# Kernel optimization log

Hardware: AMD Instinct MI355X
Metric: run time of the kernel (lower is better)

Reference implementation:

```python
import jax, jax.numpy as jnp
import numpy as np

N_NODES = 100000
N_EDGES = 1600000

def setup_inputs() -> dict:
    key = jax.random.key(0)
    ks = jax.random.split(key, 6)
    x = jax.random.normal(ks[0], (N_NODES, 128), dtype=jnp.float32)
    edge_index = jax.random.randint(ks[1], (2, N_EDGES), 0, N_NODES, dtype=jnp.int64)
    edge_weight = jax.random.uniform(ks[2], (N_EDGES,), dtype=jnp.float32)
    # kaiming-uniform-like init for weights, zeros for biases (as in reset_parameters)
    bound1 = float(np.sqrt(6.0 / 128))
    W1 = jax.random.uniform(ks[3], (128, 128), minval=-bound1, maxval=bound1, dtype=jnp.float32)
    b1 = jnp.zeros((128,), dtype=jnp.float32)
    W2 = jax.random.uniform(ks[4], (128, 64), minval=-bound1, maxval=bound1, dtype=jnp.float32)
    b2 = jnp.zeros((64,), dtype=jnp.float32)
    return {"x": x, "edge_index": edge_index, "edge_weight": edge_weight,
            "W1": W1, "b1": b1, "W2": W2, "b2": b2}

def _gcn_conv(x, src, dst, ew, W, b):
    support = x @ W                      # [N, F_out] dense GEMM
    msgs = ew[:, None] * support[src]    # [E, F_out] gather + scale (spmm values)
    out = jax.ops.segment_sum(msgs, dst, num_segments=N_NODES)  # scatter-add
    return out + b

def reference(x, edge_index, edge_weight, W1, b1, W2, b2):
    dst, src = edge_index[0], edge_index[1]  # adj[dst, src] = edge_weight
    h = _gcn_conv(x, src, dst, edge_weight, W1, b1)
    h = jax.nn.relu(h)
    out = _gcn_conv(h, src, dst, edge_weight, W2, b2)
    return out
```

## Files before the change

### kernel.cpp

```cpp
#include <hip/hip_runtime.h>

#define N_NODES 100000
#define N_EDGES 1600000
#define NB 391
#define PAD 16
#define SC_EPB 2048
#define SC_BLOCKS ((N_EDGES + SC_EPB - 1) / SC_EPB)
#define LDA 136
#define NTILES ((N_NODES + 127) / 128)

typedef unsigned int uint32;
typedef __attribute__((ext_vector_type(8))) short bf16x8;
typedef __attribute__((ext_vector_type(4))) float f32x4;

__device__ __forceinline__ uint32 bf16_rne(float f) {
    uint32 u = __float_as_uint(f);
    return (u + 0x7fffu + ((u >> 16) & 1u)) >> 16;
}
__device__ __forceinline__ uint32 pack_bf16x2(float lo, float hi) {
    return bf16_rne(lo) | (bf16_rne(hi) << 16);
}
__device__ __forceinline__ float bf16_lo(uint32 u) { return __uint_as_float(u << 16); }
__device__ __forceinline__ float bf16_hi(uint32 u) { return __uint_as_float(u & 0xFFFF0000u); }

__global__ __launch_bounds__(256) void conv_x(const float* __restrict__ x,
                                              uint32* __restrict__ xb) {
    const int t = blockIdx.x * 256 + threadIdx.x;
    if (t >= N_NODES * 64) return;
    const float2 v = ((const float2*)x)[t];
    xb[t] = pack_bf16x2(v.x, v.y);
}

__global__ __launch_bounds__(256) void conv_w(const float* __restrict__ W1,
                                              const float* __restrict__ W2,
                                              uint32* __restrict__ w1tb,
                                              uint32* __restrict__ w2tb) {
    const int t = blockIdx.x * 256 + threadIdx.x;
    if (t < 128 * 64) {
        const int n = t >> 6, kk = t & 63;
        w1tb[t] = pack_bf16x2(W1[(2 * kk) * 128 + n], W1[(2 * kk + 1) * 128 + n]);
    } else if (t < 128 * 64 + 64 * 64) {
        const int u = t - 128 * 64;
        const int n = u >> 6, kk = u & 63;
        w2tb[u] = pack_bf16x2(W2[(2 * kk) * 64 + n], W2[(2 * kk + 1) * 64 + n]);
    }
}

__global__ __launch_bounds__(256) void bucket_hist(const int* __restrict__ dst,
                                                   int* __restrict__ bktCnt) {
    __shared__ int h[NB];
    for (int i = threadIdx.x; i < NB; i += 256) h[i] = 0;
    __syncthreads();
    for (int e = blockIdx.x * 256 + threadIdx.x; e < N_EDGES; e += NB * 256)
        atomicAdd(&h[dst[e] >> 8], 1);
    __syncthreads();
    for (int i = threadIdx.x; i < NB; i += 256)
        if (h[i]) atomicAdd(&bktCnt[i * PAD], h[i]);
}

__global__ __launch_bounds__(512) void bucket_scan(const int* __restrict__ bktCnt,
                                                   int* __restrict__ bBase,
                                                   int* __restrict__ bCur,
                                                   int* __restrict__ offs) {
    __shared__ int s[512];
    const int t = threadIdx.x;
    int v = (t < NB) ? bktCnt[t * PAD] : 0;
    s[t] = v;
    __syncthreads();
#pragma unroll
    for (int off = 1; off < 512; off <<= 1) {
        int u = (t >= off) ? s[t - off] : 0;
        __syncthreads();
        s[t] += u;
        __syncthreads();
    }
    if (t < NB) {
        const int excl = s[t] - v;
        bBase[t] = excl;
        bCur[t * PAD] = excl;
    }
    if (t == 0) {
        bBase[NB] = N_EDGES;
        offs[N_NODES] = N_EDGES;
    }
}

__global__ __launch_bounds__(256) void bucket_scatter2(const int* __restrict__ dst,
                                                       const int* __restrict__ src,
                                                       const float* __restrict__ ew,
                                                       int* __restrict__ bCur,
                                                       int2* __restrict__ bucketed) {
    __shared__ int h[NB];
    __shared__ int cur[NB];
    const int base = blockIdx.x * SC_EPB;
    const int end  = min(base + SC_EPB, N_EDGES);

    for (int i = threadIdx.x; i < NB; i += 256) h[i] = 0;
    __syncthreads();
    for (int e = base + threadIdx.x; e < end; e += 256)
        atomicAdd(&h[dst[e] >> 8], 1);
    __syncthreads();
    for (int i = threadIdx.x; i < NB; i += 256) {
        const int c = h[i];
        cur[i] = c ? atomicAdd(&bCur[i * PAD], c) : 0;
    }
    __syncthreads();
    for (int e = base + threadIdx.x; e < end; e += 256) {
        const int d = dst[e];
        const int p = atomicAdd(&cur[d >> 8], 1);
        bucketed[p] = make_int2(src[e] | ((d & 255) << 17), __float_as_int(ew[e]));
    }
}

__global__ __launch_bounds__(256) void bucket_csr(const int2* __restrict__ bucketed,
                                                  const int* __restrict__ bBase,
                                                  int* __restrict__ offs,
                                                  int2* __restrict__ csr_ef) {
    __shared__ int sdeg[256];
    __shared__ int lcur[256];
    const int b   = blockIdx.x;
    const int t   = threadIdx.x;
    const int beg = bBase[b], end = bBase[b + 1];

    sdeg[t] = 0;
    __syncthreads();
    for (int j = beg + t; j < end; j += 256)
        atomicAdd(&sdeg[(bucketed[j].x >> 17) & 255], 1);
    __syncthreads();
    const int mydeg = sdeg[t];
#pragma unroll
    for (int off = 1; off < 256; off <<= 1) {
        int u = (t >= off) ? sdeg[t - off] : 0;
        __syncthreads();
        sdeg[t] += u;
        __syncthreads();
    }
    const int excl = sdeg[t] - mydeg;
    lcur[t] = excl;
    const int node = b * 256 + t;
    if (node < N_NODES) offs[node] = beg + excl;
    __syncthreads();

    for (int j = beg + t; j < end; j += 256) {
        const int2 v = bucketed[j];
        const int dl = (v.x >> 17) & 255;
        const int p  = beg + atomicAdd(&lcur[dl], 1);
        csr_ef[p] = make_int2(v.x & 0x1FFFF, v.y);
    }
}

template <int FEAT>
__global__ __launch_bounds__(256) void aggregate(const void* __restrict__ featv,
                                                 const int* __restrict__ offs,
                                                 const int2* __restrict__ csr_ef,
                                                 const float* __restrict__ bias,
                                                 void* __restrict__ outv) {
    const int n    = (blockIdx.x * 256 + threadIdx.x) >> 6;
    const int lane = threadIdx.x & 63;
    if (n >= N_NODES) return;
    const int beg = offs[n], end = offs[n + 1];
    const uint4* feat = (const uint4*)featv;

    float a0 = 0.f, a1 = 0.f, a2 = 0.f, a3 = 0.f;
    float a4 = 0.f, a5 = 0.f, a6 = 0.f, a7 = 0.f;

    if constexpr (FEAT == 128) {
        const int g  = lane >> 4;
        const int f8 = lane & 15;

        for (int j = beg + g; j < end; j += 8) {
            {
                const int2 e = csr_ef[j];
                const uint4 r = feat[(unsigned)(e.x * 16 + f8)];
                const float w = __int_as_float(e.y);
                a0 += w * bf16_lo(r.x); a1 += w * bf16_hi(r.x);
                a2 += w * bf16_lo(r.y); a3 += w * bf16_hi(r.y);
                a4 += w * bf16_lo(r.z); a5 += w * bf16_hi(r.z);
                a6 += w * bf16_lo(r.w); a7 += w * bf16_hi(r.w);
            }
            if (j + 4 < end) {
                const int2 e = csr_ef[j + 4];
                const uint4 r = feat[(unsigned)(e.x * 16 + f8)];
                const float w = __int_as_float(e.y);
                a0 += w * bf16_lo(r.x); a1 += w * bf16_hi(r.x);
                a2 += w * bf16_lo(r.y); a3 += w * bf16_hi(r.y);
                a4 += w * bf16_lo(r.z); a5 += w * bf16_hi(r.z);
                a6 += w * bf16_lo(r.w); a7 += w * bf16_hi(r.w);
            }
        }

        a0 += __shfl_xor(a0, 16); a1 += __shfl_xor(a1, 16);
        a2 += __shfl_xor(a2, 16); a3 += __shfl_xor(a3, 16);
        a4 += __shfl_xor(a4, 16); a5 += __shfl_xor(a5, 16);
        a6 += __shfl_xor(a6, 16); a7 += __shfl_xor(a7, 16);
        a0 += __shfl_xor(a0, 32); a1 += __shfl_xor(a1, 32);
        a2 += __shfl_xor(a2, 32); a3 += __shfl_xor(a3, 32);
        a4 += __shfl_xor(a4, 32); a5 += __shfl_xor(a5, 32);
        a6 += __shfl_xor(a6, 32); a7 += __shfl_xor(a7, 32);

        if (g == 0) {
            uint4 p;
            p.x = pack_bf16x2(a0, a1);
            p.y = pack_bf16x2(a2, a3);
            p.z = pack_bf16x2(a4, a5);
            p.w = pack_bf16x2(a6, a7);
            ((uint4*)outv)[(size_t)n * 16 + f8] = p;
        }
    } else {
        const int g  = lane >> 3;
        const int f4 = lane & 7;

        for (int j = beg + g; j < end; j += 16) {
            {
                const int2 e = csr_ef[j];
                const uint4 r = feat[(unsigned)(e.x * 8 + f4)];
                const float w = __int_as_float(e.y);
                a0 += w * bf16_lo(r.x); a1 += w * bf16_hi(r.x);
                a2 += w * bf16_lo(r.y); a3 += w * bf16_hi(r.y);
                a4 += w * bf16_lo(r.z); a5 += w * bf16_hi(r.z);
                a6 += w * bf16_lo(r.w); a7 += w * bf16_hi(r.w);
            }
            if (j + 8 < end) {
                const int2 e = csr_ef[j + 8];
                const uint4 r = feat[(unsigned)(e.x * 8 + f4)];
                const float w = __int_as_float(e.y);
                a0 += w * bf16_lo(r.x); a1 += w * bf16_hi(r.x);
                a2 += w * bf16_lo(r.y); a3 += w * bf16_hi(r.y);
                a4 += w * bf16_lo(r.z); a5 += w * bf16_hi(r.z);
                a6 += w * bf16_lo(r.w); a7 += w * bf16_hi(r.w);
            }
        }

        a0 += __shfl_xor(a0, 8);  a1 += __shfl_xor(a1, 8);
        a2 += __shfl_xor(a2, 8);  a3 += __shfl_xor(a3, 8);
        a4 += __shfl_xor(a4, 8);  a5 += __shfl_xor(a5, 8);
        a6 += __shfl_xor(a6, 8);  a7 += __shfl_xor(a7, 8);
        a0 += __shfl_xor(a0, 16); a1 += __shfl_xor(a1, 16);
        a2 += __shfl_xor(a2, 16); a3 += __shfl_xor(a3, 16);
        a4 += __shfl_xor(a4, 16); a5 += __shfl_xor(a5, 16);
        a6 += __shfl_xor(a6, 16); a7 += __shfl_xor(a7, 16);
        a0 += __shfl_xor(a0, 32); a1 += __shfl_xor(a1, 32);
        a2 += __shfl_xor(a2, 32); a3 += __shfl_xor(a3, 32);
        a4 += __shfl_xor(a4, 32); a5 += __shfl_xor(a5, 32);
        a6 += __shfl_xor(a6, 32); a7 += __shfl_xor(a7, 32);

        if (g == 0) {
            const float4* b4 = (const float4*)bias;
            const float4 bA = b4[f4 * 2];
            const float4 bB = b4[f4 * 2 + 1];
            float4 o0 = make_float4(a0 + bA.x, a1 + bA.y, a2 + bA.z, a3 + bA.w);
            float4 o1 = make_float4(a4 + bB.x, a5 + bB.y, a6 + bB.z, a7 + bB.w);
            ((float4*)outv)[(size_t)n * 16 + f4 * 2]     = o0;
            ((float4*)outv)[(size_t)n * 16 + f4 * 2 + 1] = o1;
        }
    }
}

__global__ __launch_bounds__(512) void gemm_fused(const uint32* __restrict__ aggPb,
                                                  const uint32* __restrict__ w1tb,
                                                  const float* __restrict__ b1,
                                                  const uint32* __restrict__ w2tb,
                                                  uint32* __restrict__ sup2b, int N) {
    __shared__ __align__(16) short As[128 * LDA];
    __shared__ __align__(16) short W1s[128 * LDA];
    __shared__ __align__(16) short W2s[64 * LDA];
    __shared__ __align__(16) short Ts[128 * LDA];

    const int tid = threadIdx.x;

    for (int i = tid; i < 128 * 16; i += 512)
        *(uint4*)&W1s[(i >> 4) * LDA + (i & 15) * 8] = ((const uint4*)w1tb)[i];
    for (int i = tid; i < 64 * 16; i += 512)
        *(uint4*)&W2s[(i >> 4) * LDA + (i & 15) * 8] = ((const uint4*)w2tb)[i];

    const int wave = tid >> 6;
    const int lane = tid & 63;
    const int m    = lane & 15;
    const int quad = lane >> 4;
    const int rowbase = (wave & 3) * 32;
    const int colbase = (wave >> 2) * 64;

    float b1r[4];
#pragma unroll
    for (int ct = 0; ct < 4; ++ct) b1r[ct] = b1[colbase + ct * 16 + m];

    for (int tile = blockIdx.x; tile < NTILES; tile += gridDim.x) {
        const int row0 = tile * 128;
        __syncthreads();

#pragma unroll
        for (int i = 0; i < 4; ++i) {
            const int idx = i * 512 + tid;
            const int row = idx >> 4, c4 = idx & 15;
            const int grow = row0 + row;
            uint4 v = make_uint4(0u, 0u, 0u, 0u);
            if (grow < N) v = ((const uint4*)aggPb)[(size_t)grow * 16 + c4];
            *(uint4*)&As[row * LDA + c4 * 8] = v;
        }
        __syncthreads();

        bf16x8 afrag[2][4];
#pragma unroll
        for (int ss = 0; ss < 2; ++ss)
#pragma unroll
            for (int ch = 0; ch < 4; ++ch)
                afrag[ss][ch] = *(const bf16x8*)&As[(rowbase + ss * 16 + m) * LDA + ch * 32 + quad * 8];

        f32x4 acc[2][4];
#pragma unroll
        for (int ss = 0; ss < 2; ++ss)
#pragma unroll
            for (int ct = 0; ct < 4; ++ct) acc[ss][ct] = (f32x4){0.f, 0.f, 0.f, 0.f};

#pragma unroll
        for (int ct = 0; ct < 4; ++ct) {
            bf16x8 bfr[4];
#pragma unroll
            for (int ch = 0; ch < 4; ++ch)
                bfr[ch] = *(const bf16x8*)&W1s[(colbase + ct * 16 + m) * LDA + ch * 32 + quad * 8];
#pragma unroll
            for (int ss = 0; ss < 2; ++ss)
#pragma unroll
                for (int ch = 0; ch < 4; ++ch)
                    acc[ss][ct] = __builtin_amdgcn_mfma_f32_16x16x32_bf16(
                        afrag[ss][ch], bfr[ch], acc[ss][ct], 0, 0, 0);
        }

#pragma unroll
        for (int ss = 0; ss < 2; ++ss)
#pragma unroll
            for (int ct = 0; ct < 4; ++ct)
#pragma unroll
                for (int r = 0; r < 4; ++r) {
                    const float v = fmaxf(acc[ss][ct][r] + b1r[ct], 0.f);
                    const int row = rowbase + ss * 16 + quad * 4 + r;
                    const int col = colbase + ct * 16 + m;
                    Ts[row * LDA + col] = (short)bf16_rne(v);
                }
        __syncthreads();

        const int rb2 = wave * 16;
        bf16x8 tfrag[4];
#pragma unroll
        for (int ch = 0; ch < 4; ++ch)
            tfrag[ch] = *(const bf16x8*)&Ts[(rb2 + m) * LDA + ch * 32 + quad * 8];

        f32x4 acc2[4];
#pragma unroll
        for (int ct = 0; ct < 4; ++ct) acc2[ct] = (f32x4){0.f, 0.f, 0.f, 0.f};
#pragma unroll
        for (int ct = 0; ct < 4; ++ct)
#pragma unroll
            for (int ch = 0; ch < 4; ++ch) {
                const bf16x8 bfr = *(const bf16x8*)&W2s[(ct * 16 + m) * LDA + ch * 32 + quad * 8];
                acc2[ct] = __builtin_amdgcn_mfma_f32_16x16x32_bf16(
                    tfrag[ch], bfr, acc2[ct], 0, 0, 0);
            }

#pragma unroll
        for (int ct = 0; ct < 4; ++ct)
#pragma unroll
            for (int r = 0; r < 4; ++r) {
                const int row = rb2 + quad * 4 + r;
                const int col = ct * 16 + m;
                As[row * LDA + col] = (short)bf16_rne(acc2[ct][r]);
            }
        __syncthreads();
#pragma unroll
        for (int i = 0; i < 2; ++i) {
            const int idx = i * 512 + tid;
            const int row = idx >> 3, c4 = idx & 7;
            if (row0 + row < N)
                ((uint4*)sup2b)[(size_t)(row0 + row) * 8 + c4] = *(uint4*)&As[row * LDA + c4 * 8];
        }
    }
}

extern "C" void kernel_launch(void* const* d_in, const int* in_sizes, int n_in,
                              void* d_out, int out_size, void* d_ws, size_t ws_size,
                              hipStream_t stream) {
    const float* x  = (const float*)d_in[0];
    const int*   ei = (const int*)d_in[1];
    const float* ew = (const float*)d_in[2];
    const float* W1 = (const float*)d_in[3];
    const float* b1 = (const float*)d_in[4];
    const float* W2 = (const float*)d_in[5];
    const float* b2 = (const float*)d_in[6];
    float* out = (float*)d_out;

    const int* dstIdx = ei;
    const int* srcIdx = ei + N_EDGES;

    uint32* xb      = (uint32*)d_ws;
    uint32* aggPb   = xb + (size_t)N_NODES * 64;
    uint32* w1tb    = aggPb + (size_t)N_NODES * 64;
    uint32* w2tb    = w1tb + 128 * 64;
    int2*   csr_ef  = (int2*)(xb + (size_t)N_NODES * 64 + (size_t)N_NODES * 128);
    int*    bktCnt  = (int*)(csr_ef + N_EDGES);
    int*    bCur    = bktCnt + NB * PAD;
    int*    bBase   = bCur + NB * PAD;
    int*    offs    = bBase + NB + 1;
    int2*   bucketed = (int2*)aggPb;
    uint32* sup2b   = xb;

    (void)hipMemsetAsync(bktCnt, 0, (size_t)NB * PAD * sizeof(int), stream);
    conv_x<<<(N_NODES * 64 + 255) / 256, 256, 0, stream>>>(x, xb);
    conv_w<<<48, 256, 0, stream>>>(W1, W2, w1tb, w2tb);

    bucket_hist<<<NB, 256, 0, stream>>>(dstIdx, bktCnt);
    bucket_scan<<<1, 512, 0, stream>>>(bktCnt, bBase, bCur, offs);
    bucket_scatter2<<<SC_BLOCKS, 256, 0, stream>>>(dstIdx, srcIdx, ew, bCur, bucketed);
    bucket_csr<<<NB, 256, 0, stream>>>(bucketed, bBase, offs, csr_ef);

    aggregate<128><<<(N_NODES * 64) / 256, 256, 0, stream>>>(xb, offs, csr_ef,
                                                             nullptr, aggPb);
    gemm_fused<<<256, 512, 0, stream>>>(aggPb, w1tb, b1, w2tb, sup2b, N_NODES);

    aggregate<64><<<(N_NODES * 64) / 256, 256, 0, stream>>>(sup2b, offs, csr_ef,
                                                            b2, out);
}
```

Before: 337.2 us.

## Build CSR with global degree atomics and direct scatter; unroll aggregate gather by four

Replaces the two-level bucketed CSR construction (bucket histogram, bucket scan, bucket scatter, per-bucket local sort) with a per-node degree count via global atomics, a three-kernel multi-block prefix scan, and a direct atomic-cursor edge scatter into CSR. The intent is to drop the intermediate bucketed buffer and one full pass over the edges. In exchange it relies on 1.6M global atomics on random addresses, and edge order within each node becomes nondeterministic. The 128-wide aggregate loop is also unrolled from two to four edges per iteration to keep more gathers in flight.

Measured after the change: 428.6 us. 27.1% more time.

```diff
diff --git a/kernel.cpp b/kernel.cpp
--- a/kernel.cpp
+++ b/kernel.cpp
@@ -2,12 +2,10 @@
 
 #define N_NODES 100000
 #define N_EDGES 1600000
-#define NB 391
-#define PAD 16
-#define SC_EPB 2048
-#define SC_BLOCKS ((N_EDGES + SC_EPB - 1) / SC_EPB)
 #define LDA 136
 #define NTILES ((N_NODES + 127) / 128)
+#define SCAN_B 512
+#define SCAN_NB ((N_NODES + SCAN_B - 1) / SCAN_B)
 
 typedef unsigned int uint32;
 typedef __attribute__((ext_vector_type(8))) short bf16x8;
@@ -46,107 +44,75 @@
     }
 }
 
-__global__ __launch_bounds__(256) void bucket_hist(const int* __restrict__ dst,
-                                                   int* __restrict__ bktCnt) {
-    __shared__ int h[NB];
-    for (int i = threadIdx.x; i < NB; i += 256) h[i] = 0;
-    __syncthreads();
-    for (int e = blockIdx.x * 256 + threadIdx.x; e < N_EDGES; e += NB * 256)
-        atomicAdd(&h[dst[e] >> 8], 1);
-    __syncthreads();
-    for (int i = threadIdx.x; i < NB; i += 256)
-        if (h[i]) atomicAdd(&bktCnt[i * PAD], h[i]);
-}
-
-__global__ __launch_bounds__(512) void bucket_scan(const int* __restrict__ bktCnt,
-                                                   int* __restrict__ bBase,
-                                                   int* __restrict__ bCur,
-                                                   int* __restrict__ offs) {
-    __shared__ int s[512];
+__global__ __launch_bounds__(256) void deg_count(const int* __restrict__ dst,
+                                                 int* __restrict__ deg) {
+    const int t = blockIdx.x * 256 + threadIdx.x;
+    const int2 d2 = ((const int2*)dst)[t];
+    atomicAdd(&deg[d2.x], 1);
+    atomicAdd(&deg[d2.y], 1);
+}
+
+__global__ __launch_bounds__(SCAN_B) void scan_blk(const int* __restrict__ deg,
+                                                   int* __restrict__ offs,
+                                                   int* __restrict__ partials) {
+    __shared__ int s[SCAN_B];
     const int t = threadIdx.x;
-    int v = (t < NB) ? bktCnt[t * PAD] : 0;
+    const int i = blockIdx.x * SCAN_B + t;
+    const int v = (i < N_NODES) ? deg[i] : 0;
     s[t] = v;
     __syncthreads();
 #pragma unroll
-    for (int off = 1; off < 512; off <<= 1) {
-        int u = (t >= off) ? s[t - off] : 0;
+    for (int off = 1; off < SCAN_B; off <<= 1) {
+        const int u = (t >= off) ? s[t - off] : 0;
         __syncthreads();
         s[t] += u;
         __syncthreads();
     }
-    if (t < NB) {
-        const int excl = s[t] - v;
-        bBase[t] = excl;
-        bCur[t * PAD] = excl;
-    }
-    if (t == 0) {
-        bBase[NB] = N_EDGES;
-        offs[N_NODES] = N_EDGES;
-    }
-}
-
-__global__ __launch_bounds__(256) void bucket_scatter2(const int* __restrict__ dst,
-                                                       const int* __restrict__ src,
-                                                       const float* __restrict__ ew,
-                                                       int* __restrict__ bCur,
-                                                       int2* __restrict__ bucketed) {
-    __shared__ int h[NB];
-    __shared__ int cur[NB];
-    const int base = blockIdx.x * SC_EPB;
-    const int end  = min(base + SC_EPB, N_EDGES);
-
-    for (int i = threadIdx.x; i < NB; i += 256) h[i] = 0;
+    if (i < N_NODES) offs[i] = s[t] - v;
+    if (t == SCAN_B - 1) partials[blockIdx.x] = s[t];
+}
+
+__global__ __launch_bounds__(256) void scan_top(int* __restrict__ partials) {
+    __shared__ int s[256];
+    const int t = threadIdx.x;
+    const int v = (t < SCAN_NB) ? partials[t] : 0;
+    s[t] = v;
     __syncthreads();
-    for (int e = base + threadIdx.x; e < end; e += 256)
-        atomicAdd(&h[dst[e] >> 8], 1);
-    __syncthreads();
-    for (int i = threadIdx.x; i < NB; i += 256) {
-        const int c = h[i];
-        cur[i] = c ? atomicAdd(&bCur[i * PAD], c) : 0;
-    }
-    __syncthreads();
-    for (int e = base + threadIdx.x; e < end; e += 256) {
-        const int d = dst[e];
-        const int p = atomicAdd(&cur[d >> 8], 1);
-        bucketed[p] = make_int2(src[e] | ((d & 255) << 17), __float_as_int(ew[e]));
-    }
-}
-
-__global__ __launch_bounds__(256) void bucket_csr(const int2* __restrict__ bucketed,
-                                                  const int* __restrict__ bBase,
-                                                  int* __restrict__ offs,
-                                                  int2* __restrict__ csr_ef) {
-    __shared__ int sdeg[256];
-    __shared__ int lcur[256];
-    const int b   = blockIdx.x;
-    const int t   = threadIdx.x;
-    const int beg = bBase[b], end = bBase[b + 1];
-
-    sdeg[t] = 0;
-    __syncthreads();
-    for (int j = beg + t; j < end; j += 256)
-        atomicAdd(&sdeg[(bucketed[j].x >> 17) & 255], 1);
-    __syncthreads();
-    const int mydeg = sdeg[t];
 #pragma unroll
     for (int off = 1; off < 256; off <<= 1) {
-        int u = (t >= off) ? sdeg[t - off] : 0;
-        __syncthreads();
-        sdeg[t] += u;
-        __syncthreads();
-    }
-    const int excl = sdeg[t] - mydeg;
-    lcur[t] = excl;
-    const int node = b * 256 + t;
-    if (node < N_NODES) offs[node] = beg + excl;
-    __syncthreads();
-
-    for (int j = beg + t; j < end; j += 256) {
-        const int2 v = bucketed[j];
-        const int dl = (v.x >> 17) & 255;
-        const int p  = beg + atomicAdd(&lcur[dl], 1);
-        csr_ef[p] = make_int2(v.x & 0x1FFFF, v.y);
-    }
+        const int u = (t >= off) ? s[t - off] : 0;
+        __syncthreads();
+        s[t] += u;
+        __syncthreads();
+    }
+    if (t < SCAN_NB) partials[t] = s[t] - v;
+}
+
+__global__ __launch_bounds__(SCAN_B) void scan_add(int* __restrict__ offs,
+                                                   const int* __restrict__ partials,
+                                                   int* __restrict__ cur) {
+    const int i = blockIdx.x * SCAN_B + threadIdx.x;
+    if (i < N_NODES) {
+        const int o = offs[i] + partials[blockIdx.x];
+        offs[i] = o;
+        cur[i]  = o;
+    }
+    if (i == 0) offs[N_NODES] = N_EDGES;
+}
+
+__global__ __launch_bounds__(256) void edge_scatter(const int* __restrict__ dst,
+                                                    const int* __restrict__ src,
+                                                    const float* __restrict__ ew,
+                                                    int* __restrict__ cur,
+                                                    int2* __restrict__ csr_ef) {
+    const int t = blockIdx.x * 256 + threadIdx.x;
+    const int2   d2 = ((const int2*)dst)[t];
+    const int2   s2 = ((const int2*)src)[t];
+    const float2 w2 = ((const float2*)ew)[t];
+    const int p0 = atomicAdd(&cur[d2.x], 1);
+    csr_ef[p0] = make_int2(s2.x, __float_as_int(w2.x));
+    const int p1 = atomicAdd(&cur[d2.y], 1);
+    csr_ef[p1] = make_int2(s2.y, __float_as_int(w2.y));
 }
 
 template <int FEAT>
@@ -168,24 +134,19 @@
         const int g  = lane >> 4;
         const int f8 = lane & 15;
 
-        for (int j = beg + g; j < end; j += 8) {
-            {
-                const int2 e = csr_ef[j];
-                const uint4 r = feat[(unsigned)(e.x * 16 + f8)];
-                const float w = __int_as_float(e.y);
-                a0 += w * bf16_lo(r.x); a1 += w * bf16_hi(r.x);
-                a2 += w * bf16_lo(r.y); a3 += w * bf16_hi(r.y);
-                a4 += w * bf16_lo(r.z); a5 += w * bf16_hi(r.z);
-                a6 += w * bf16_lo(r.w); a7 += w * bf16_hi(r.w);
-            }
-            if (j + 4 < end) {
-                const int2 e = csr_ef[j + 4];
-                const uint4 r = feat[(unsigned)(e.x * 16 + f8)];
-                const float w = __int_as_float(e.y);
-                a0 += w * bf16_lo(r.x); a1 += w * bf16_hi(r.x);
-                a2 += w * bf16_lo(r.y); a3 += w * bf16_hi(r.y);
-                a4 += w * bf16_lo(r.z); a5 += w * bf16_hi(r.z);
-                a6 += w * bf16_lo(r.w); a7 += w * bf16_hi(r.w);
+        for (int j = beg + g; j < end; j += 16) {
+#pragma unroll
+            for (int u = 0; u < 4; ++u) {
+                const int jj = j + u * 4;
+                if (u == 0 || jj < end) {
+                    const int2 e = csr_ef[jj];
+                    const uint4 r = feat[(unsigned)(e.x * 16 + f8)];
+                    const float w = __int_as_float(e.y);
+                    a0 += w * bf16_lo(r.x); a1 += w * bf16_hi(r.x);
+                    a2 += w * bf16_lo(r.y); a3 += w * bf16_hi(r.y);
+                    a4 += w * bf16_lo(r.z); a5 += w * bf16_hi(r.z);
+                    a6 += w * bf16_lo(r.w); a7 += w * bf16_hi(r.w);
+                }
             }
         }
 
@@ -395,22 +356,22 @@
     uint32* aggPb   = xb + (size_t)N_NODES * 64;
     uint32* w1tb    = aggPb + (size_t)N_NODES * 64;
     uint32* w2tb    = w1tb + 128 * 64;
-    int2*   csr_ef  = (int2*)(xb + (size_t)N_NODES * 64 + (size_t)N_NODES * 128);
-    int*    bktCnt  = (int*)(csr_ef + N_EDGES);
-    int*    bCur    = bktCnt + NB * PAD;
-    int*    bBase   = bCur + NB * PAD;
-    int*    offs    = bBase + NB + 1;
-    int2*   bucketed = (int2*)aggPb;
+    int2*   csr_ef  = (int2*)(w2tb + 64 * 64);
+    int*    deg     = (int*)(csr_ef + N_EDGES);
+    int*    cur     = deg + N_NODES;
+    int*    partials = cur + N_NODES;
+    int*    offs    = partials + 256;
     uint32* sup2b   = xb;
 
-    (void)hipMemsetAsync(bktCnt, 0, (size_t)NB * PAD * sizeof(int), stream);
+    (void)hipMemsetAsync(deg, 0, (size_t)N_NODES * sizeof(int), stream);
     conv_x<<<(N_NODES * 64 + 255) / 256, 256, 0, stream>>>(x, xb);
     conv_w<<<48, 256, 0, stream>>>(W1, W2, w1tb, w2tb);
 
-    bucket_hist<<<NB, 256, 0, stream>>>(dstIdx, bktCnt);
-    bucket_scan<<<1, 512, 0, stream>>>(bktCnt, bBase, bCur, offs);
-    bucket_scatter2<<<SC_BLOCKS, 256, 0, stream>>>(dstIdx, srcIdx, ew, bCur, bucketed);
-    bucket_csr<<<NB, 256, 0, stream>>>(bucketed, bBase, offs, csr_ef);
+    deg_count<<<N_EDGES / 2 / 256, 256, 0, stream>>>(dstIdx, deg);
+    scan_blk<<<SCAN_NB, SCAN_B, 0, stream>>>(deg, offs, partials);
+    scan_top<<<1, 256, 0, stream>>>(partials);
+    scan_add<<<SCAN_NB, SCAN_B, 0, stream>>>(offs, partials, cur);
+    edge_scatter<<<N_EDGES / 2 / 256, 256, 0, stream>>>(dstIdx, srcIdx, ew, cur, csr_ef);
 
     aggregate<128><<<(N_NODES * 64) / 256, 256, 0, stream>>>(xb, offs, csr_ef,
                                                              nullptr, aggPb);
```
